# Kernel optimization log

Hardware: AMD Instinct MI355X
Metric: run time of the kernel (lower is better)

Reference implementation:

```python
import jax, jax.numpy as jnp
import numpy as np

INF = 1e10
PROBS_THRESHOLD = 0.7
ALPHA = 3.0
DICE_EPS = 1e-6


def edt2d(mask0):
    """Exact Euclidean distance transform of a 2D slice.
    mask0: [H, W] bool, True where the pixel is background (value == 0).
    Returns per-pixel distance to nearest background pixel (0 on background),
    matching scipy.ndimage.distance_transform_edt on the complementary image.
    Separable decomposition: 1D column pass then min-plus row pass.
    """
    H, W = mask0.shape
    ii = jnp.arange(H, dtype=jnp.float32)
    # column pass: g[i, j] = min_{i': mask0[i', j]} |i - i'|   -> [H, W]
    d_col = jnp.abs(ii[:, None] - ii[None, :])                 # [H(i), H(i')]
    g = jnp.min(jnp.where(mask0[None, :, :], d_col[:, :, None], INF), axis=1)
    jj = jnp.arange(W, dtype=jnp.float32)
    dj2 = (jj[:, None] - jj[None, :]) ** 2                     # [W(j), W(j')]
    # row pass: edt^2[i, j] = min_{j'} g[i, j']^2 + (j - j')^2
    edt2 = jnp.min(g[:, None, :] ** 2 + dj2[None, :, :], axis=2)  # [H, W]
    return jnp.sqrt(edt2)


def _combined_distance(y_threshed):
    """y_threshed: [B, 1, D, H, W] float 0/1. Returns combined clipped EDT map."""
    x = y_threshed[:, 0]                                        # [B, D, H, W]
    B, D, H, W = x.shape
    edt_slices = jax.vmap(jax.vmap(lambda s, v: edt2d(s == v), in_axes=(0, None)),
                          in_axes=(0, None))
    dst = edt_slices(x, 1.0)   # distance_transform_edt(slice): bg where slice==0
    inv = edt_slices(x, 0.0)   # wait: see below
    # scipy edt(img): nonzero pixels -> dist to nearest zero => background mask is img==0
    # so dst uses mask0 = (s == 0); inverted uses mask0 = (1 - s == 0) i.e. (s == 1)
    dst = jax.vmap(jax.vmap(lambda s: edt2d(s == 0.0)))(x)      # [B, D, H, W]
    inv = jax.vmap(jax.vmap(lambda s: edt2d(s == 1.0)))(x)      # [B, D, H, W]
    combined = dst + inv
    # get_glioma_indices: first/last slice containing foreground
    present = jnp.any(x > 0, axis=(2, 3))                       # [B, D]
    first = jnp.argmax(present, axis=1)                         # [B]
    last = D - 1 - jnp.argmax(present[:, ::-1], axis=1)         # [B]
    dvec = jnp.arange(D)
    in_range = (dvec[None, :] >= first[:, None]) & (dvec[None, :] <= last[:, None])
    combined = jnp.where(in_range[:, :, None, None], combined, 0.0)
    # thresh_mode == 'max': thresh_val = max of dst of the LAST processed slice
    dst_last = jax.vmap(lambda d, l: d[l])(dst, last)           # [B, H, W]
    thresh = jnp.max(dst_last, axis=(1, 2))                     # [B]
    combined = jnp.minimum(combined, thresh[:, None, None, None])
    return combined[:, None]                                    # [B, 1, D, H, W]


def dice_coefficient(y_pred, y_true):
    inter = jnp.sum(y_pred * y_true)
    return (2.0 * inter) / (jnp.sum(y_pred) + jnp.sum(y_true) + DICE_EPS)


def reference(y_pred, y_true):
    y_threshed = jax.lax.stop_gradient((y_pred > PROBS_THRESHOLD).astype(jnp.float32))
    combined = _combined_distance(y_threshed)                   # [B, 1, D, H, W]
    mask = y_true > 0
    mean_sel = jnp.sum(jnp.where(mask, combined, 0.0)) / jnp.sum(mask)
    distance_loss = jnp.abs(1.0 - mean_sel)
    dice_loss = 1.0 - dice_coefficient(y_pred, y_true)
    return dice_loss + ALPHA * distance_loss


def setup_inputs() -> dict:
    key = jax.random.key(0)
    k1, k2 = jax.random.split(key)
    B, C, D, H, W = 2, 1, 64, 128, 128
    y_pred = jax.random.uniform(k1, (B, C, D, H, W), dtype=jnp.float32)
    y_true = jax.random.randint(k2, (B, C, D, H, W), 0, 2).astype(jnp.float32)
    return {"y_pred": y_pred, "y_true": y_true}
```

## Files before the change

### kernel.cpp

```cpp
#include <hip/hip_runtime.h>
#include <hip/hip_bf16.h>

#define BATCH 2
#define DEPTH 64
#define HH 128
#define WW 128
#define SLICES (BATCH*DEPTH)
#define SLICE_ELEMS (HH*WW)
#define NELEM (SLICES*SLICE_ELEMS)
#define NV4 (NELEM/4)
#define RBLK 1024

__global__ __launch_bounds__(256) void edt_kernel(const float* __restrict__ y_pred,
        float* __restrict__ combined, float* __restrict__ maxdst_blocks)
{
    __shared__ unsigned int tmp[HH][WW];
    __shared__ float wred[4];
    int blk = blockIdx.x;
    int s  = blk >> 1;
    int hb = blk & 1;
    int t  = threadIdx.x;
    const float* base = y_pred + (size_t)s * SLICE_ELEMS;

    if (t < WW) {
        unsigned mm[4];
        #pragma unroll
        for (int g = 0; g < 4; ++g) {
            unsigned acc = 0u;
            #pragma unroll
            for (int ii = 0; ii < 32; ++ii) {
                int r = g*32 + ii;
                acc |= (base[r*WW + t] > 0.7f ? 1u : 0u) << ii;
            }
            mm[g] = acc;
        }
        int dd = 300, di = 300;
        #pragma unroll
        for (int g = 0; g < 4; ++g) {
            unsigned mg = mm[g];
            #pragma unroll
            for (int ii = 0; ii < 32; ++ii) {
                int i = g*32 + ii;
                int fg = (mg >> ii) & 1;
                dd = fg ? dd + 1 : 0;
                di = fg ? 0 : di + 1;
                tmp[i][t] = ((unsigned)di << 16) | (unsigned)dd;
            }
        }
        dd = 300; di = 300;
        #pragma unroll
        for (int g = 3; g >= 0; --g) {
            unsigned mg = mm[g];
            #pragma unroll
            for (int ii = 31; ii >= 0; --ii) {
                int i = g*32 + ii;
                int fg = (mg >> ii) & 1;
                dd = fg ? dd + 1 : 0;
                di = fg ? 0 : di + 1;
                unsigned p = tmp[i][t];
                int fd = min((int)(p & 0xFFFFu), dd);
                int fi = min((int)(p >> 16), di);
                unsigned sd = (fd >= 128) ? 0xFFFFu : (unsigned)(fd*fd);
                unsigned si = (fi >= 128) ? 0xFFFFu : (unsigned)(fi*fi);
                tmp[i][t] = (si << 16) | sd;
            }
        }
    }
    __syncthreads();

    int j  = t & (WW-1);
    int ri = t >> 7;
    float dmax = 0.0f;
    float* cbase = combined + (size_t)s * SLICE_ELEMS;
    for (int it = 0; it < 32; ++it) {
        int i = hb*64 + it*2 + ri;
        unsigned p = tmp[i][j];
        unsigned rawd = p & 0xFFFFu, rawi = p >> 16;
        int cfg = (rawi == 0u);
        unsigned rsel = cfg ? rawd : rawi;
        float bd = (rsel == 0xFFFFu) ? 1e20f : (float)rsel;
        for (int r = 1; r < WW; ++r) {
            float r2 = (float)(r*r);
            if (__all(r2 >= bd)) break;
            int jl = j - r, jr = j + r;
            unsigned pl = tmp[i][jl & (WW-1)];
            unsigned pr = tmp[i][jr & (WW-1)];
            unsigned sl = cfg ? (pl & 0xFFFFu) : (pl >> 16);
            unsigned sr = cfg ? (pr & 0xFFFFu) : (pr >> 16);
            float gl = (sl == 0xFFFFu) ? 1e20f : (float)sl;
            float gr = (sr == 0xFFFFu) ? 1e20f : (float)sr;
            gl = (jl >= 0) ? gl : 3e38f;
            gr = (jr < WW) ? gr : 3e38f;
            bd = fminf(bd, r2 + fminf(gl, gr));
        }
        float dco = sqrtf(bd);
        cbase[i*WW + j] = dco;
        if (cfg) dmax = fmaxf(dmax, dco);
    }
    for (int off = 32; off > 0; off >>= 1)
        dmax = fmaxf(dmax, __shfl_down(dmax, off));
    if ((t & 63) == 0) wred[t >> 6] = dmax;
    __syncthreads();
    if (t == 0)
        maxdst_blocks[s*2 + hb] = fmaxf(fmaxf(wred[0], wred[1]), fmaxf(wred[2], wred[3]));
}

__global__ __launch_bounds__(64) void range_kernel(const float* __restrict__ maxdst_blocks,
        int* __restrict__ firstlast, float* __restrict__ thresh)
{
    int b = threadIdx.x;
    if (b < BATCH) {
        int f = 0, l = DEPTH-1;
        for (int d = DEPTH-1; d >= 0; --d) {
            int s = b*DEPTH + d;
            if (fmaxf(maxdst_blocks[2*s], maxdst_blocks[2*s+1]) > 0.0f) f = d;
        }
        for (int d = 0; d < DEPTH; ++d) {
            int s = b*DEPTH + d;
            if (fmaxf(maxdst_blocks[2*s], maxdst_blocks[2*s+1]) > 0.0f) l = d;
        }
        firstlast[b] = f;
        firstlast[BATCH + b] = l;
        int sl = b*DEPTH + l;
        thresh[b] = fmaxf(maxdst_blocks[2*sl], maxdst_blocks[2*sl+1]);
    }
}

__global__ __launch_bounds__(256) void reduce_kernel(const float4* __restrict__ yp4,
        const float4* __restrict__ yt4, const float4* __restrict__ cb4,
        const int* __restrict__ firstlast, const float* __restrict__ thresh,
        float* __restrict__ partials)
{
    float v0=0.f, v1=0.f, v2=0.f, v3=0.f, v4=0.f;
    for (int i4 = blockIdx.x*256 + threadIdx.x; i4 < NV4; i4 += RBLK*256) {
        int idx = i4 << 2;
        int b = idx >> 20;
        int d = (idx >> 14) & (DEPTH-1);
        float4 p = yp4[i4];
        float4 q = yt4[i4];
        float4 cc = cb4[i4];
        float th = thresh[b];
        bool inr = (d >= firstlast[b]) && (d <= firstlast[BATCH + b]);
        float c0 = fminf(inr ? cc.x : 0.0f, th);
        float c1 = fminf(inr ? cc.y : 0.0f, th);
        float c2 = fminf(inr ? cc.z : 0.0f, th);
        float c3 = fminf(inr ? cc.w : 0.0f, th);
        float m0 = (q.x > 0.f) ? 1.f : 0.f;
        float m1 = (q.y > 0.f) ? 1.f : 0.f;
        float m2 = (q.z > 0.f) ? 1.f : 0.f;
        float m3 = (q.w > 0.f) ? 1.f : 0.f;
        v0 += p.x*q.x + p.y*q.y + p.z*q.z + p.w*q.w;
        v1 += p.x + p.y + p.z + p.w;
        v2 += q.x + q.y + q.z + q.w;
        v3 += m0*c0 + m1*c1 + m2*c2 + m3*c3;
        v4 += m0 + m1 + m2 + m3;
    }
    for (int off = 32; off > 0; off >>= 1) {
        v0 += __shfl_down(v0, off);
        v1 += __shfl_down(v1, off);
        v2 += __shfl_down(v2, off);
        v3 += __shfl_down(v3, off);
        v4 += __shfl_down(v4, off);
    }
    __shared__ float wsum[4][5];
    int wv = threadIdx.x >> 6;
    if ((threadIdx.x & 63) == 0) {
        wsum[wv][0]=v0; wsum[wv][1]=v1; wsum[wv][2]=v2; wsum[wv][3]=v3; wsum[wv][4]=v4;
    }
    __syncthreads();
    if (threadIdx.x == 0) {
        #pragma unroll
        for (int qd = 0; qd < 5; ++qd)
            partials[qd*RBLK + blockIdx.x] = wsum[0][qd]+wsum[1][qd]+wsum[2][qd]+wsum[3][qd];
    }
}

__global__ __launch_bounds__(1024) void final_kernel(const float* __restrict__ partials,
                                                     float* __restrict__ out)
{
    int t = threadIdx.x;
    double l0 = (double)partials[0*RBLK + t];
    double l1 = (double)partials[1*RBLK + t];
    double l2 = (double)partials[2*RBLK + t];
    double l3 = (double)partials[3*RBLK + t];
    double l4 = (double)partials[4*RBLK + t];
    for (int off = 32; off > 0; off >>= 1) {
        l0 += __shfl_down(l0, off);
        l1 += __shfl_down(l1, off);
        l2 += __shfl_down(l2, off);
        l3 += __shfl_down(l3, off);
        l4 += __shfl_down(l4, off);
    }
    __shared__ double ds[16][5];
    int wv = t >> 6;
    if ((t & 63) == 0) { ds[wv][0]=l0; ds[wv][1]=l1; ds[wv][2]=l2; ds[wv][3]=l3; ds[wv][4]=l4; }
    __syncthreads();
    if (t == 0) {
        double inter=0, spred=0, strue=0, sel=0, cnt=0;
        for (int w = 0; w < 16; ++w) {
            inter += ds[w][0]; spred += ds[w][1]; strue += ds[w][2];
            sel   += ds[w][3]; cnt   += ds[w][4];
        }
        double dice = 2.0 * inter / (spred + strue + 1e-6);
        double mean_sel = sel / cnt;
        double loss = (1.0 - dice) + 3.0 * fabs(1.0 - mean_sel);
        out[0] = (float)loss;
    }
}

extern "C" void kernel_launch(void* const* d_in, const int* in_sizes, int n_in,
                              void* d_out, int out_size, void* d_ws, size_t ws_size,
                              hipStream_t stream) {
    const float* y_pred = (const float*)d_in[0];
    const float* y_true = (const float*)d_in[1];
    float* out = (float*)d_out;
    char* ws = (char*)d_ws;

    float* thresh        = (float*)ws;
    int*   firstlast     = (int*)(ws + 64);
    float* maxdst_blocks = (float*)(ws + 128);
    float* partials      = (float*)(ws + 2048);
    float* combined      = (float*)(ws + 32768);

    edt_kernel<<<SLICES*2, 256, 0, stream>>>(y_pred, combined, maxdst_blocks);
    range_kernel<<<1, 64, 0, stream>>>(maxdst_blocks, firstlast, thresh);
    reduce_kernel<<<RBLK, 256, 0, stream>>>((const float4*)y_pred, (const float4*)y_true,
                                            (const float4*)combined, firstlast, thresh, partials);
    final_kernel<<<1, 1024, 0, stream>>>(partials, out);
}
```

Baseline: 106.5 us.

## Merge EDT slice halves, parallelize column scans, fold range/final into reduce

The EDT kernel now handles one whole slice per 512-thread block instead of two half-slice blocks. Thresholding is spread across all threads, and the forward and backward column scans run concurrently in separate shared buffers, then combine in a parallel pass. The range and final kernels are removed: the reduce kernel computes first/last slice and threshold with a wave ballot, and accumulates with double atomics plus a last-block-done counter. This cuts launch count and serial column work, at the cost of more shared memory per block (about 130KB), fewer blocks for the EDT stage, and atomics whose order is nondeterministic.

```diff
diff --git a/kernel.cpp b/kernel.cpp
--- a/kernel.cpp
+++ b/kernel.cpp
@@ -11,59 +11,78 @@
 #define NV4 (NELEM/4)
 #define RBLK 1024
 
-__global__ __launch_bounds__(256) void edt_kernel(const float* __restrict__ y_pred,
-        float* __restrict__ combined, float* __restrict__ maxdst_blocks)
+__global__ __launch_bounds__(512) void edt_kernel(const float* __restrict__ y_pred,
+        float* __restrict__ combined, float* __restrict__ maxdst,
+        double* __restrict__ acc, int* __restrict__ counter)
 {
-    __shared__ unsigned int tmp[HH][WW];
-    __shared__ float wred[4];
-    int blk = blockIdx.x;
-    int s  = blk >> 1;
-    int hb = blk & 1;
-    int t  = threadIdx.x;
+    __shared__ unsigned mm_sh[WW][4];
+    __shared__ unsigned tmpF[HH][WW];
+    __shared__ unsigned tmpB[HH][WW];
+    __shared__ float wred[8];
+    int s = blockIdx.x;
+    int t = threadIdx.x;
+    if (s == 0 && t < 6) {
+        if (t < 5) acc[t] = 0.0; else counter[0] = 0;
+    }
     const float* base = y_pred + (size_t)s * SLICE_ELEMS;
 
+    {
+        int col = t & (WW-1);
+        int g = t >> 7;
+        unsigned accm = 0u;
+        #pragma unroll
+        for (int ii = 0; ii < 32; ++ii) {
+            int r = g*32 + ii;
+            accm |= (base[r*WW + col] > 0.7f ? 1u : 0u) << ii;
+        }
+        mm_sh[col][g] = accm;
+    }
+    __syncthreads();
+
     if (t < WW) {
-        unsigned mm[4];
+        int dd = 300, di = 300;
         #pragma unroll
         for (int g = 0; g < 4; ++g) {
-            unsigned acc = 0u;
-            #pragma unroll
-            for (int ii = 0; ii < 32; ++ii) {
-                int r = g*32 + ii;
-                acc |= (base[r*WW + t] > 0.7f ? 1u : 0u) << ii;
-            }
-            mm[g] = acc;
-        }
-        int dd = 300, di = 300;
-        #pragma unroll
-        for (int g = 0; g < 4; ++g) {
-            unsigned mg = mm[g];
+            unsigned mg = mm_sh[t][g];
             #pragma unroll
             for (int ii = 0; ii < 32; ++ii) {
                 int i = g*32 + ii;
                 int fg = (mg >> ii) & 1;
                 dd = fg ? dd + 1 : 0;
                 di = fg ? 0 : di + 1;
-                tmp[i][t] = ((unsigned)di << 16) | (unsigned)dd;
+                tmpF[i][t] = ((unsigned)di << 16) | (unsigned)dd;
             }
         }
-        dd = 300; di = 300;
+    } else if (t < 2*WW) {
+        int c = t - WW;
+        int dd = 300, di = 300;
         #pragma unroll
         for (int g = 3; g >= 0; --g) {
-            unsigned mg = mm[g];
+            unsigned mg = mm_sh[c][g];
             #pragma unroll
             for (int ii = 31; ii >= 0; --ii) {
                 int i = g*32 + ii;
                 int fg = (mg >> ii) & 1;
                 dd = fg ? dd + 1 : 0;
                 di = fg ? 0 : di + 1;
-                unsigned p = tmp[i][t];
-                int fd = min((int)(p & 0xFFFFu), dd);
-                int fi = min((int)(p >> 16), di);
-                unsigned sd = (fd >= 128) ? 0xFFFFu : (unsigned)(fd*fd);
-                unsigned si = (fi >= 128) ? 0xFFFFu : (unsigned)(fi*fi);
-                tmp[i][t] = (si << 16) | sd;
+                tmpB[i][c] = ((unsigned)di << 16) | (unsigned)dd;
             }
+        }
+    }
+    __syncthreads();
+
+    {
+        unsigned* F = &tmpF[0][0];
+        unsigned* B = &tmpB[0][0];
+        #pragma unroll
+        for (int k = 0; k < 32; ++k) {
+            int c = k*512 + t;
+            unsigned pf = F[c], pb = B[c];
+            int fd = min((int)(pf & 0xFFFFu), (int)(pb & 0xFFFFu));
+            int fi = min((int)(pf >> 16),     (int)(pb >> 16));
+            unsigned sd = (fd >= 128) ? 0xFFFFu : (unsigned)(fd*fd);
+            unsigned si = (fi >= 128) ? 0xFFFFu : (unsigned)(fi*fi);
+            F[c] = (si << 16) | sd;
         }
     }
     __syncthreads();
@@ -73,8 +92,8 @@
     float dmax = 0.0f;
     float* cbase = combined + (size_t)s * SLICE_ELEMS;
     for (int it = 0; it < 32; ++it) {
-        int i = hb*64 + it*2 + ri;
-        unsigned p = tmp[i][j];
+        int i = it*4 + ri;
+        unsigned p = tmpF[i][j];
         unsigned rawd = p & 0xFFFFu, rawi = p >> 16;
         int cfg = (rawi == 0u);
         unsigned rsel = cfg ? rawd : rawi;
@@ -83,8 +102,8 @@
             float r2 = (float)(r*r);
             if (__all(r2 >= bd)) break;
             int jl = j - r, jr = j + r;
-            unsigned pl = tmp[i][jl & (WW-1)];
-            unsigned pr = tmp[i][jr & (WW-1)];
+            unsigned pl = tmpF[i][jl & (WW-1)];
+            unsigned pr = tmpF[i][jr & (WW-1)];
             unsigned sl = cfg ? (pl & 0xFFFFu) : (pl >> 16);
             unsigned sr = cfg ? (pr & 0xFFFFu) : (pr >> 16);
             float gl = (sl == 0xFFFFu) ? 1e20f : (float)sl;
@@ -101,46 +120,48 @@
         dmax = fmaxf(dmax, __shfl_down(dmax, off));
     if ((t & 63) == 0) wred[t >> 6] = dmax;
     __syncthreads();
-    if (t == 0)
-        maxdst_blocks[s*2 + hb] = fmaxf(fmaxf(wred[0], wred[1]), fmaxf(wred[2], wred[3]));
-}
-
-__global__ __launch_bounds__(64) void range_kernel(const float* __restrict__ maxdst_blocks,
-        int* __restrict__ firstlast, float* __restrict__ thresh)
-{
-    int b = threadIdx.x;
-    if (b < BATCH) {
-        int f = 0, l = DEPTH-1;
-        for (int d = DEPTH-1; d >= 0; --d) {
-            int s = b*DEPTH + d;
-            if (fmaxf(maxdst_blocks[2*s], maxdst_blocks[2*s+1]) > 0.0f) f = d;
-        }
-        for (int d = 0; d < DEPTH; ++d) {
-            int s = b*DEPTH + d;
-            if (fmaxf(maxdst_blocks[2*s], maxdst_blocks[2*s+1]) > 0.0f) l = d;
-        }
-        firstlast[b] = f;
-        firstlast[BATCH + b] = l;
-        int sl = b*DEPTH + l;
-        thresh[b] = fmaxf(maxdst_blocks[2*sl], maxdst_blocks[2*sl+1]);
+    if (t == 0) {
+        float mx = 0.0f;
+        #pragma unroll
+        for (int w = 0; w < 8; ++w) mx = fmaxf(mx, wred[w]);
+        maxdst[s] = mx;
     }
 }
 
 __global__ __launch_bounds__(256) void reduce_kernel(const float4* __restrict__ yp4,
         const float4* __restrict__ yt4, const float4* __restrict__ cb4,
-        const int* __restrict__ firstlast, const float* __restrict__ thresh,
-        float* __restrict__ partials)
+        const float* __restrict__ maxdst,
+        double* __restrict__ acc, int* __restrict__ counter, float* __restrict__ out)
 {
+    __shared__ int sh_f[2], sh_l[2];
+    __shared__ float sh_t[2];
+    int t = threadIdx.x;
+    if (t < 128) {
+        int b = t >> 6, d = t & 63;
+        float mx = maxdst[b*DEPTH + d];
+        unsigned long long mask = __ballot(mx > 0.0f);
+        int f = 0, l = DEPTH-1;
+        if (mask) {
+            f = __ffsll(mask) - 1;
+            l = 63 - __clzll(mask);
+        }
+        if (d == 0) { sh_f[b] = f; sh_l[b] = l; }
+        if (d == l) sh_t[b] = mx;
+    }
+    __syncthreads();
+    int f0 = sh_f[0], l0 = sh_l[0], f1 = sh_f[1], l1 = sh_l[1];
+    float th0 = sh_t[0], th1 = sh_t[1];
+
     float v0=0.f, v1=0.f, v2=0.f, v3=0.f, v4=0.f;
-    for (int i4 = blockIdx.x*256 + threadIdx.x; i4 < NV4; i4 += RBLK*256) {
+    for (int i4 = blockIdx.x*256 + t; i4 < NV4; i4 += RBLK*256) {
         int idx = i4 << 2;
         int b = idx >> 20;
         int d = (idx >> 14) & (DEPTH-1);
         float4 p = yp4[i4];
         float4 q = yt4[i4];
         float4 cc = cb4[i4];
-        float th = thresh[b];
-        bool inr = (d >= firstlast[b]) && (d <= firstlast[BATCH + b]);
+        bool inr = b ? (d >= f1 && d <= l1) : (d >= f0 && d <= l0);
+        float th = b ? th1 : th0;
         float c0 = fminf(inr ? cc.x : 0.0f, th);
         float c1 = fminf(inr ? cc.y : 0.0f, th);
         float c2 = fminf(inr ? cc.z : 0.0f, th);
@@ -163,48 +184,30 @@
         v4 += __shfl_down(v4, off);
     }
     __shared__ float wsum[4][5];
-    int wv = threadIdx.x >> 6;
-    if ((threadIdx.x & 63) == 0) {
+    int wv = t >> 6;
+    if ((t & 63) == 0) {
         wsum[wv][0]=v0; wsum[wv][1]=v1; wsum[wv][2]=v2; wsum[wv][3]=v3; wsum[wv][4]=v4;
     }
     __syncthreads();
-    if (threadIdx.x == 0) {
-        #pragma unroll
-        for (int qd = 0; qd < 5; ++qd)
-            partials[qd*RBLK + blockIdx.x] = wsum[0][qd]+wsum[1][qd]+wsum[2][qd]+wsum[3][qd];
-    }
-}
-
-__global__ __launch_bounds__(1024) void final_kernel(const float* __restrict__ partials,
-                                                     float* __restrict__ out)
-{
-    int t = threadIdx.x;
-    double l0 = (double)partials[0*RBLK + t];
-    double l1 = (double)partials[1*RBLK + t];
-    double l2 = (double)partials[2*RBLK + t];
-    double l3 = (double)partials[3*RBLK + t];
-    double l4 = (double)partials[4*RBLK + t];
-    for (int off = 32; off > 0; off >>= 1) {
-        l0 += __shfl_down(l0, off);
-        l1 += __shfl_down(l1, off);
-        l2 += __shfl_down(l2, off);
-        l3 += __shfl_down(l3, off);
-        l4 += __shfl_down(l4, off);
-    }
-    __shared__ double ds[16][5];
-    int wv = t >> 6;
-    if ((t & 63) == 0) { ds[wv][0]=l0; ds[wv][1]=l1; ds[wv][2]=l2; ds[wv][3]=l3; ds[wv][4]=l4; }
-    __syncthreads();
     if (t == 0) {
-        double inter=0, spred=0, strue=0, sel=0, cnt=0;
-        for (int w = 0; w < 16; ++w) {
-            inter += ds[w][0]; spred += ds[w][1]; strue += ds[w][2];
-            sel   += ds[w][3]; cnt   += ds[w][4];
-        }
-        double dice = 2.0 * inter / (spred + strue + 1e-6);
-        double mean_sel = sel / cnt;
-        double loss = (1.0 - dice) + 3.0 * fabs(1.0 - mean_sel);
-        out[0] = (float)loss;
+        atomicAdd(&acc[0], (double)(wsum[0][0]+wsum[1][0]+wsum[2][0]+wsum[3][0]));
+        atomicAdd(&acc[1], (double)(wsum[0][1]+wsum[1][1]+wsum[2][1]+wsum[3][1]));
+        atomicAdd(&acc[2], (double)(wsum[0][2]+wsum[1][2]+wsum[2][2]+wsum[3][2]));
+        atomicAdd(&acc[3], (double)(wsum[0][3]+wsum[1][3]+wsum[2][3]+wsum[3][3]));
+        atomicAdd(&acc[4], (double)(wsum[0][4]+wsum[1][4]+wsum[2][4]+wsum[3][4]));
+        __threadfence();
+        int old = atomicAdd(counter, 1);
+        if (old == RBLK - 1) {
+            __threadfence();
+            double inter = atomicAdd(&acc[0], 0.0);
+            double spred = atomicAdd(&acc[1], 0.0);
+            double strue = atomicAdd(&acc[2], 0.0);
+            double sel   = atomicAdd(&acc[3], 0.0);
+            double cnt   = atomicAdd(&acc[4], 0.0);
+            double dice = 2.0 * inter / (spred + strue + 1e-6);
+            double mean_sel = sel / cnt;
+            out[0] = (float)((1.0 - dice) + 3.0 * fabs(1.0 - mean_sel));
+        }
     }
 }
 
@@ -216,15 +219,12 @@
     float* out = (float*)d_out;
     char* ws = (char*)d_ws;
 
-    float* thresh        = (float*)ws;
-    int*   firstlast     = (int*)(ws + 64);
-    float* maxdst_blocks = (float*)(ws + 128);
-    float* partials      = (float*)(ws + 2048);
-    float* combined      = (float*)(ws + 32768);
-
-    edt_kernel<<<SLICES*2, 256, 0, stream>>>(y_pred, combined, maxdst_blocks);
-    range_kernel<<<1, 64, 0, stream>>>(maxdst_blocks, firstlast, thresh);
+    float*  maxdst   = (float*)(ws + 128);
+    double* acc      = (double*)(ws + 1024);
+    int*    counter  = (int*)(ws + 1088);
+    float*  combined = (float*)(ws + 32768);
+
+    edt_kernel<<<SLICES, 512, 0, stream>>>(y_pred, combined, maxdst, acc, counter);
     reduce_kernel<<<RBLK, 256, 0, stream>>>((const float4*)y_pred, (const float4*)y_true,
-                                            (const float4*)combined, firstlast, thresh, partials);
-    final_kernel<<<1, 1024, 0, stream>>>(partials, out);
+                                            (const float4*)combined, maxdst, acc, counter, out);
 }
```

Result: slower. 158.0 us (+48.4%).
